# Kernel optimization log

Hardware: AMD Instinct MI355X
Metric: run time of the kernel (lower is better)

The kernel has to match this reference:

```python
import jax, jax.numpy as jnp
import numpy as np

DIM = 1024
HEADS = 16
HEAD_DIM = DIM // HEADS
HIDDEN = 4 * DIM
EPS = 1e-5
SCALE = HEAD_DIM ** -0.5


def _ln(x, g, b):
    m = jnp.mean(x, axis=-1, keepdims=True)
    v = jnp.mean(jnp.square(x - m), axis=-1, keepdims=True)
    return (x - m) * jax.lax.rsqrt(v + EPS) * g + b


def setup_inputs() -> dict:
    key = jax.random.key(0)
    ks = jax.random.split(key, 12)
    B, L = 4, 1024
    s = lambda fan: 1.0 / np.sqrt(fan)
    return {
        "x": jax.random.normal(ks[0], (B, L, DIM), jnp.float32),
        "skip": jax.random.normal(ks[1], (B, L, DIM), jnp.float32),
        "skip_w": jax.random.normal(ks[2], (2 * DIM, DIM), jnp.float32) * s(2 * DIM),
        "skip_b": jnp.zeros((DIM,), jnp.float32),
        "ln1_g": jnp.ones((DIM,), jnp.float32),
        "ln1_b": jnp.zeros((DIM,), jnp.float32),
        "qkv_w": jax.random.normal(ks[3], (DIM, 3 * DIM), jnp.float32) * s(DIM),
        "proj_w": jax.random.normal(ks[4], (DIM, DIM), jnp.float32) * s(DIM),
        "proj_b": jnp.zeros((DIM,), jnp.float32),
        "ln2_g": jnp.ones((DIM,), jnp.float32),
        "ln2_b": jnp.zeros((DIM,), jnp.float32),
        "fc1_w": jax.random.normal(ks[5], (DIM, HIDDEN), jnp.float32) * s(DIM),
        "fc1_b": jnp.zeros((HIDDEN,), jnp.float32),
        "fc2_w": jax.random.normal(ks[6], (HIDDEN, DIM), jnp.float32) * s(HIDDEN),
        "fc2_b": jnp.zeros((DIM,), jnp.float32),
        "ln3_g": jnp.ones((DIM,), jnp.float32),
        "ln3_b": jnp.zeros((DIM,), jnp.float32),
    }


def reference(x, skip, skip_w, skip_b, ln1_g, ln1_b, qkv_w, proj_w, proj_b,
              ln2_g, ln2_b, fc1_w, fc1_b, fc2_w, fc2_b, ln3_g, ln3_b):
    B, L, C = x.shape
    # skip-concat + linear + norm1
    x = jnp.concatenate([x, skip], axis=2) @ skip_w + skip_b
    x = _ln(x, ln1_g, ln1_b)
    # attention (naive: full [B,H,L,L] score matrix, as in source)
    qkv = (x @ qkv_w).reshape(B, L, 3, HEADS, HEAD_DIM)
    qkv = jnp.transpose(qkv, (2, 0, 3, 1, 4))  # [3,B,H,L,D]
    q, k, v = qkv[0], qkv[1], qkv[2]
    attn = jax.nn.softmax(jnp.einsum("bhld,bhmd->bhlm", q, k) * SCALE, axis=-1)
    o = jnp.einsum("bhlm,bhmd->bhld", attn, v)
    o = jnp.transpose(o, (0, 2, 1, 3)).reshape(B, L, C) @ proj_w + proj_b
    x = x + o
    x = _ln(x, ln2_g, ln2_b)
    # MLP with exact (erf) GELU, matching torch default
    h = jax.nn.gelu(x @ fc1_w + fc1_b, approximate=False)
    x = x + (h @ fc2_w + fc2_b)
    x = _ln(x, ln3_g, ln3_b)
    return x
```

## Files before the change

### kernel.cpp

```cpp
#include <hip/hip_runtime.h>

typedef float f32x4 __attribute__((ext_vector_type(4)));
typedef short s16x8 __attribute__((ext_vector_type(8)));

#define MFMA16(a, b, c) __builtin_amdgcn_mfma_f32_16x16x32_bf16(a, b, c, 0, 0, 0)
#define SCALE 0.125f

__device__ __forceinline__ unsigned short f2bf(float f) {
    unsigned u = __float_as_uint(f);
    u = u + 0x7FFFu + ((u >> 16) & 1u);
    return (unsigned short)(u >> 16);
}

__device__ __forceinline__ float fast_gelu(float x) {
    float u = 1.5957691216f * (x + 0.044715f * x * x * x);
    u = fminf(u, 30.f);
    const float e = __expf(u);
    return x * e / (e + 1.f);
}

typedef const __attribute__((address_space(1))) void* gptr_t;
typedef __attribute__((address_space(3))) void* lptr_t;
__device__ __forceinline__ void gload16(const void* g, void* l) {
    __builtin_amdgcn_global_load_lds((gptr_t)g, (lptr_t)l, 16, 0, 0);
}

__global__ __launch_bounds__(256) void cvt_cat(const float* __restrict__ x,
                                               const float* __restrict__ skip,
                                               unsigned short* __restrict__ out) {
    const size_t i = ((size_t)blockIdx.x * 256 + threadIdx.x) * 8;
    const int r = (int)(i >> 11);
    const int c = (int)(i & 2047);
    const float* src = (c < 1024) ? (x + (size_t)r * 1024 + c)
                                  : (skip + (size_t)r * 1024 + (c - 1024));
    float4 v0 = *(const float4*)src;
    float4 v1 = *(const float4*)(src + 4);
    s16x8 o;
    o[0] = f2bf(v0.x); o[1] = f2bf(v0.y); o[2] = f2bf(v0.z); o[3] = f2bf(v0.w);
    o[4] = f2bf(v1.x); o[5] = f2bf(v1.y); o[6] = f2bf(v1.z); o[7] = f2bf(v1.w);
    *(s16x8*)(out + i) = o;
}

__global__ __launch_bounds__(256) void wt_tr(const float* __restrict__ in,
                                             unsigned short* __restrict__ out,
                                             int R, int C) {
    __shared__ unsigned short tile[64][72];
    const int nct = C >> 6;
    const int tr = blockIdx.x / nct, tc = blockIdx.x % nct;
    const int t = threadIdx.x;
    const int r = t >> 2, c0 = (t & 3) << 4;
    const float* src = in + (size_t)(tr * 64 + r) * C + tc * 64 + c0;
#pragma unroll
    for (int j = 0; j < 16; j += 4) {
        float4 v = *(const float4*)(src + j);
        tile[r][c0 + j]     = f2bf(v.x);
        tile[r][c0 + j + 1] = f2bf(v.y);
        tile[r][c0 + j + 2] = f2bf(v.z);
        tile[r][c0 + j + 3] = f2bf(v.w);
    }
    __syncthreads();
    const int oc = t >> 2, r0 = (t & 3) << 4;
    s16x8 o0, o1;
#pragma unroll
    for (int j = 0; j < 8; ++j) { o0[j] = tile[r0 + j][oc]; o1[j] = tile[r0 + 8 + j][oc]; }
    unsigned short* dst = out + (size_t)(tc * 64 + oc) * R + tr * 64 + r0;
    *(s16x8*)dst = o0;
    *(s16x8*)(dst + 8) = o1;
}

__global__ __launch_bounds__(256) void v_transpose(const unsigned short* __restrict__ qkv,
                                                   unsigned short* __restrict__ vt) {
    __shared__ unsigned short tile[64][72];
    const int bh = blockIdx.x >> 4, lt = blockIdx.x & 15;
    const int b = bh >> 4, h = bh & 15;
    const int t = threadIdx.x;
    const int r = t >> 2, c0 = (t & 3) << 4;
    const unsigned short* src =
        qkv + (size_t)(b * 1024 + lt * 64 + r) * 3072 + 2048 + h * 64 + c0;
    s16x8 v0 = *(const s16x8*)src;
    s16x8 v1 = *(const s16x8*)(src + 8);
#pragma unroll
    for (int j = 0; j < 8; ++j) { tile[r][c0 + j] = v0[j]; tile[r][c0 + 8 + j] = v1[j]; }
    __syncthreads();
    const int d = t >> 2, l0 = (t & 3) << 4;
    s16x8 o0, o1;
#pragma unroll
    for (int j = 0; j < 8; ++j) { o0[j] = tile[l0 + j][d]; o1[j] = tile[l0 + 8 + j][d]; }
    unsigned short* dst = vt + (size_t)bh * 65536 + (size_t)d * 1024 + lt * 64 + l0;
    *(s16x8*)dst = o0;
    *(s16x8*)(dst + 8) = o1;
}

__global__ __launch_bounds__(256) void ln_kernel(const float* __restrict__ in,
                                                 const float* __restrict__ g,
                                                 const float* __restrict__ bb,
                                                 float* __restrict__ outf,
                                                 unsigned short* __restrict__ outb) {
    const int row = blockIdx.x;
    const int t = threadIdx.x;
    const float4 v = ((const float4*)(in + (size_t)row * 1024))[t];
    float s = v.x + v.y + v.z + v.w;
    float ss = v.x * v.x + v.y * v.y + v.z * v.z + v.w * v.w;
#pragma unroll
    for (int off = 1; off < 64; off <<= 1) {
        s += __shfl_xor(s, off, 64);
        ss += __shfl_xor(ss, off, 64);
    }
    __shared__ float red[8];
    const int wave = t >> 6, lane = t & 63;
    if (lane == 0) { red[wave] = s; red[4 + wave] = ss; }
    __syncthreads();
    s = red[0] + red[1] + red[2] + red[3];
    ss = red[4] + red[5] + red[6] + red[7];
    const float mean = s * 0.0009765625f;
    const float var = ss * 0.0009765625f - mean * mean;
    const float rstd = rsqrtf(var + 1e-5f);
    const float4 gv = ((const float4*)g)[t];
    const float4 bv = ((const float4*)bb)[t];
    float4 ov;
    ov.x = (v.x - mean) * rstd * gv.x + bv.x;
    ov.y = (v.y - mean) * rstd * gv.y + bv.y;
    ov.z = (v.z - mean) * rstd * gv.z + bv.z;
    ov.w = (v.w - mean) * rstd * gv.w + bv.w;
    if (outf) ((float4*)(outf + (size_t)row * 1024))[t] = ov;
    if (outb) {
        ushort4 ob;
        ob.x = f2bf(ov.x); ob.y = f2bf(ov.y); ob.z = f2bf(ov.z); ob.w = f2bf(ov.w);
        *(ushort4*)(outb + (size_t)row * 1024 + t * 4) = ob;
    }
}

template <int EPI>
__global__ __launch_bounds__(256) void gemm_bt(const unsigned short* __restrict__ A,
                                               const unsigned short* __restrict__ Bt,
                                               void* __restrict__ outp,
                                               const float* __restrict__ bias,
                                               const float* __restrict__ resid,
                                               int M, int N, int K) {
    __shared__ __align__(16) unsigned short sA[2][128 * 32];
    __shared__ __align__(16) unsigned short sB[2][128 * 32];
    const int tid = threadIdx.x, wave = tid >> 6, lane = tid & 63;
    const int fr = lane & 15, fq = lane >> 4;
    const int nbn = N >> 7;
    const int wg = (blockIdx.x & 7) * ((int)gridDim.x >> 3) + (blockIdx.x >> 3);
    const int bm = wg / nbn, bn = wg % nbn;
    const int wm = wave >> 1, wn = wave & 1;
    const unsigned short* Ab = A + (size_t)bm * 128 * K;
    const unsigned short* Bb = Bt + (size_t)bn * 128 * K;
    const int srow = wave * 32 + (lane >> 2);
    const int scol = (lane & 3) * 8;

    f32x4 acc[4][4];
#pragma unroll
    for (int i = 0; i < 4; ++i)
#pragma unroll
        for (int j = 0; j < 4; ++j) acc[i][j] = (f32x4){0.f, 0.f, 0.f, 0.f};

    auto stage = [&](int buf, int k0) {
        const unsigned short* ga = Ab + (size_t)srow * K + k0 + scol;
        const unsigned short* gb = Bb + (size_t)srow * K + k0 + scol;
        unsigned short* la = &sA[buf][wave * 32 * 32];
        unsigned short* lb = &sB[buf][wave * 32 * 32];
        gload16(ga, la);
        gload16(ga + (size_t)16 * K, la + 16 * 32);
        gload16(gb, lb);
        gload16(gb + (size_t)16 * K, lb + 16 * 32);
    };

    const int nkt = K >> 5;
    stage(0, 0);
    for (int kt = 0; kt < nkt; ++kt) {
        __syncthreads();
        if (kt + 1 < nkt) stage((kt + 1) & 1, (kt + 1) * 32);
        const unsigned short* a0 = &sA[kt & 1][0];
        const unsigned short* b0 = &sB[kt & 1][0];
        s16x8 af[4], bf[4];
#pragma unroll
        for (int i = 0; i < 4; ++i)
            af[i] = *(const s16x8*)(a0 + (wm * 64 + i * 16 + fr) * 32 + fq * 8);
#pragma unroll
        for (int j = 0; j < 4; ++j)
            bf[j] = *(const s16x8*)(b0 + (wn * 64 + j * 16 + fr) * 32 + fq * 8);
#pragma unroll
        for (int i = 0; i < 4; ++i)
#pragma unroll
            for (int j = 0; j < 4; ++j) acc[i][j] = MFMA16(af[i], bf[j], acc[i][j]);
    }

#pragma unroll
    for (int i = 0; i < 4; ++i) {
        const int row0 = bm * 128 + wm * 64 + i * 16 + fq * 4;
#pragma unroll
        for (int j = 0; j < 4; ++j) {
            const int col = bn * 128 + wn * 64 + j * 16 + fr;
            const float bv = (EPI == 2) ? 0.f : bias[col];
#pragma unroll
            for (int r = 0; r < 4; ++r) {
                const int row = row0 + r;
                float v = acc[i][j][r] + bv;
                if (EPI == 3) v = fast_gelu(v);
                if (EPI == 1) v += resid[(size_t)row * N + col];
                if (EPI == 0 || EPI == 1)
                    ((float*)outp)[(size_t)row * N + col] = v;
                else
                    ((unsigned short*)outp)[(size_t)row * N + col] = f2bf(v);
            }
        }
    }
}

template <int EPI>
__global__ __launch_bounds__(512) void gemm256(const unsigned short* __restrict__ A,
                                               const unsigned short* __restrict__ Bt,
                                               unsigned short* __restrict__ outp,
                                               const float* __restrict__ bias,
                                               int N, int K) {
    __shared__ __align__(16) unsigned short lds[4][16384];
    const int tid = threadIdx.x, wave = tid >> 6, lane = tid & 63;
    const int fr = lane & 15, fq = lane >> 4;
    const int wm = wave >> 2, wn = wave & 3;
    const int nbn = N >> 8;
    const int wg = (blockIdx.x & 7) * ((int)gridDim.x >> 3) + (blockIdx.x >> 3);
    const int bm = wg / nbn, bn = wg % nbn;
    const unsigned short* Ab = A + (size_t)bm * 256 * K;
    const unsigned short* Bb = Bt + (size_t)bn * 256 * K;
    const int nt = K >> 5;

    f32x4 acc[8][4];
#pragma unroll
    for (int i = 0; i < 8; ++i)
#pragma unroll
        for (int n = 0; n < 4; ++n) acc[i][n] = (f32x4){0.f, 0.f, 0.f, 0.f};

    const int srow = tid >> 2;
    const int scol = (tid & 3) * 8;

    auto stage2 = [&](int tt, int s0) {
#pragma unroll
        for (int s = s0; s < s0 + 2; ++s) {
            const unsigned short* base = (s < 2) ? Ab : Bb;
            const int row = ((s & 1) << 7) + srow;
            gload16(base + (size_t)row * K + tt * 32 + scol,
                    (char*)&lds[tt & 3][0] + s * 8192 + tid * 16);
        }
    };

    stage2(0, 0); stage2(0, 2);
    stage2(1, 0); stage2(1, 2);
    stage2(2, 0); stage2(2, 2);

    for (int t = 0; t < nt; ++t) {
        __builtin_amdgcn_sched_barrier(0);
        if (t + 2 < nt)      asm volatile("s_waitcnt vmcnt(8)" ::: "memory");
        else if (t + 1 < nt) asm volatile("s_waitcnt vmcnt(4)" ::: "memory");
        else                 asm volatile("s_waitcnt vmcnt(0)" ::: "memory");
        __builtin_amdgcn_sched_barrier(0);
        __builtin_amdgcn_s_barrier();

        const unsigned short* lb = &lds[t & 3][0];
        s16x8 af[4], bfr[4];
#pragma unroll
        for (int i = 0; i < 4; ++i)
            af[i] = *(const s16x8*)(lb + (wm * 128 + i * 16 + fr) * 32 + fq * 8);
#pragma unroll
        for (int n = 0; n < 4; ++n)
            bfr[n] = *(const s16x8*)(lb + 8192 + (wn * 64 + n * 16 + fr) * 32 + fq * 8);
        if (t + 3 < nt) stage2(t + 3, 0);
        __builtin_amdgcn_s_barrier();
        __builtin_amdgcn_s_setprio(1);
#pragma unroll
        for (int i = 0; i < 4; ++i)
#pragma unroll
            for (int n = 0; n < 4; ++n) acc[i][n] = MFMA16(af[i], bfr[n], acc[i][n]);
        __builtin_amdgcn_s_setprio(0);
        __builtin_amdgcn_s_barrier();
#pragma unroll
        for (int i = 0; i < 4; ++i)
            af[i] = *(const s16x8*)(lb + (wm * 128 + 64 + i * 16 + fr) * 32 + fq * 8);
        if (t + 3 < nt) stage2(t + 3, 2);
        __builtin_amdgcn_s_barrier();
        __builtin_amdgcn_s_setprio(1);
#pragma unroll
        for (int i = 0; i < 4; ++i)
#pragma unroll
            for (int n = 0; n < 4; ++n) acc[4 + i][n] = MFMA16(af[i], bfr[n], acc[4 + i][n]);
        __builtin_amdgcn_s_setprio(0);
        __builtin_amdgcn_s_barrier();
    }

#pragma unroll
    for (int a2 = 0; a2 < 8; ++a2) {
        const int row0 = bm * 256 + wm * 128 + ((a2 >> 2) << 6) + ((a2 & 3) << 4) + fq * 4;
#pragma unroll
        for (int n = 0; n < 4; ++n) {
            const int col = bn * 256 + wn * 64 + n * 16 + fr;
            const float bv = (EPI == 3) ? bias[col] : 0.f;
#pragma unroll
            for (int r = 0; r < 4; ++r) {
                float v = acc[a2][n][r] + bv;
                if (EPI == 3) v = fast_gelu(v);
                outp[(size_t)(row0 + r) * N + col] = f2bf(v);
            }
        }
    }
}

__global__ __launch_bounds__(256) void attn_kernel(const unsigned short* __restrict__ qkv,
                                                   const unsigned short* __restrict__ vt,
                                                   unsigned short* __restrict__ o) {
    __shared__ __align__(16) unsigned short sK[2][64 * 64];
    __shared__ __align__(16) unsigned short sV[2][64 * 64];
    __shared__ __align__(16) unsigned short sP[4][16 * 64];

    const int j = blockIdx.x;
    const int xcd = j & 7, ix = j >> 3;
    const int bh = xcd * 8 + (ix >> 4);
    const int qt = ix & 15;
    const int b = bh >> 4, h = bh & 15;

    const int tid = threadIdx.x;
    const int wave = tid >> 6, lane = tid & 63;
    const int fr = lane & 15, fq = lane >> 4;

    const unsigned short* kbase = qkv + (size_t)(b * 1024) * 3072 + 1024 + h * 64;
    const unsigned short* vbase = vt + (size_t)bh * 65536;

    const int qrow0 = b * 1024 + qt * 64 + wave * 16;
    const unsigned short* qp = qkv + (size_t)(qrow0 + fr) * 3072 + h * 64;
    const s16x8 aq0 = *(const s16x8*)(qp + fq * 8);
    const s16x8 aq1 = *(const s16x8*)(qp + 32 + fq * 8);

    const f32x4 zero4 = {0.f, 0.f, 0.f, 0.f};
    float m[4], l[4];
    f32x4 oacc[4];
#pragma unroll
    for (int r = 0; r < 4; ++r) { m[r] = -1e30f; l[r] = 0.f; }
#pragma unroll
    for (int n = 0; n < 4; ++n) oacc[n] = zero4;

    auto stage = [&](int buf, int kt) {
#pragma unroll
        for (int c = 0; c < 2; ++c) {
            const int ob = tid * 16 + c * 4096;
            const int row = ob >> 7;
            const int slot = (ob >> 4) & 7;
            const int cole = ((slot ^ (row & 7)) << 3);
            gload16(kbase + (size_t)(kt * 64 + row) * 3072 + cole,
                    (char*)&sK[buf][0] + ob);
            gload16(vbase + (size_t)row * 1024 + kt * 64 + cole,
                    (char*)&sV[buf][0] + ob);
        }
    };

    unsigned short* pw = &sP[wave][0];
    const int psw = (fr & 7) << 4;

    stage(0, 0);
    for (int kt = 0; kt < 16; ++kt) {
        const int cur = kt & 1;
        __syncthreads();
        if (kt + 1 < 16) stage(cur ^ 1, kt + 1);

        const unsigned short* kb = &sK[cur][0];
        f32x4 s[4];
        __builtin_amdgcn_s_setprio(1);
#pragma unroll
        for (int n = 0; n < 4; ++n) {
            const int R = n * 16 + fr;
            const int sw = (R & 7) << 3;
            const s16x8 bk0 = *(const s16x8*)(kb + R * 64 + ((fq * 8) ^ sw));
            const s16x8 bk1 = *(const s16x8*)(kb + R * 64 + ((32 + fq * 8) ^ sw));
            s[n] = MFMA16(aq0, bk0, zero4);
            s[n] = MFMA16(aq1, bk1, s[n]);
        }
        __builtin_amdgcn_s_setprio(0);

        float mnew[4], alpha[4], rs[4];
#pragma unroll
        for (int r = 0; r < 4; ++r) {
            float t = fmaxf(fmaxf(s[0][r], s[1][r]), fmaxf(s[2][r], s[3][r])) * SCALE;
#pragma unroll
            for (int off = 1; off < 16; off <<= 1) t = fmaxf(t, __shfl_xor(t, off, 64));
            mnew[r] = fmaxf(m[r], t);
            alpha[r] = __expf(m[r] - mnew[r]);
            rs[r] = 0.f;
        }
#pragma unroll
        for (int n = 0; n < 4; ++n) {
#pragma unroll
            for (int r = 0; r < 4; ++r) {
                const float p = __expf(s[n][r] * SCALE - mnew[r]);
                rs[r] += p;
                const int prow = fq * 4 + r;
                const int pb = prow * 128 + (((n * 16 + fr) * 2) ^ ((prow & 7) << 4));
                *(unsigned short*)((char*)pw + pb) = f2bf(p);
            }
        }
#pragma unroll
        for (int r = 0; r < 4; ++r) {
            float t = rs[r];
#pragma unroll
            for (int off = 1; off < 16; off <<= 1) t += __shfl_xor(t, off, 64);
            l[r] = l[r] * alpha[r] + t;
            m[r] = mnew[r];
        }
#pragma unroll
        for (int n = 0; n < 4; ++n) {
            oacc[n][0] *= alpha[0]; oacc[n][1] *= alpha[1];
            oacc[n][2] *= alpha[2]; oacc[n][3] *= alpha[3];
        }

        const s16x8 ap0 = *(const s16x8*)((char*)pw + fr * 128 + ((fq * 16) ^ psw));
        const s16x8 ap1 = *(const s16x8*)((char*)pw + fr * 128 + ((64 + fq * 16) ^ psw));
        const unsigned short* vb = &sV[cur][0];
        __builtin_amdgcn_s_setprio(1);
#pragma unroll
        for (int n = 0; n < 4; ++n) {
            const int R = n * 16 + fr;
            const int sw = (R & 7) << 3;
            const s16x8 bv0 = *(const s16x8*)(vb + R * 64 + ((fq * 8) ^ sw));
            const s16x8 bv1 = *(const s16x8*)(vb + R * 64 + ((32 + fq * 8) ^ sw));
            oacc[n] = MFMA16(ap0, bv0, oacc[n]);
            oacc[n] = MFMA16(ap1, bv1, oacc[n]);
        }
        __builtin_amdgcn_s_setprio(0);
    }

#pragma unroll
    for (int r = 0; r < 4; ++r) {
        const float rl = 1.f / l[r];
        const int row = qrow0 + fq * 4 + r;
#pragma unroll
        for (int n = 0; n < 4; ++n) {
            const int col = h * 64 + n * 16 + fr;
            o[(size_t)row * 1024 + col] = f2bf(oacc[n][r] * rl);
        }
    }
}

extern "C" void kernel_launch(void* const* d_in, const int* in_sizes, int n_in,
                              void* d_out, int out_size, void* d_ws, size_t ws_size,
                              hipStream_t stream) {
    (void)in_sizes; (void)n_in; (void)out_size; (void)ws_size;
    const float* x      = (const float*)d_in[0];
    const float* skip   = (const float*)d_in[1];
    const float* skip_w = (const float*)d_in[2];
    const float* skip_b = (const float*)d_in[3];
    const float* ln1_g  = (const float*)d_in[4];
    const float* ln1_b  = (const float*)d_in[5];
    const float* qkv_w  = (const float*)d_in[6];
    const float* proj_w = (const float*)d_in[7];
    const float* proj_b = (const float*)d_in[8];
    const float* ln2_g  = (const float*)d_in[9];
    const float* ln2_b  = (const float*)d_in[10];
    const float* fc1_w  = (const float*)d_in[11];
    const float* fc1_b  = (const float*)d_in[12];
    const float* fc2_w  = (const float*)d_in[13];
    const float* fc2_b  = (const float*)d_in[14];
    const float* ln3_g  = (const float*)d_in[15];
    const float* ln3_b  = (const float*)d_in[16];

    char* ws = (char*)d_ws;
    const size_t MB = 1u << 20;
    unsigned short* skip_wT = (unsigned short*)(ws + 0 * MB);
    unsigned short* qkv_wT  = (unsigned short*)(ws + 4 * MB);
    unsigned short* proj_wT = (unsigned short*)(ws + 10 * MB);
    unsigned short* fc1_wT  = (unsigned short*)(ws + 12 * MB);
    unsigned short* fc2_wT  = (unsigned short*)(ws + 20 * MB);
    float* pre              = (float*)(ws + 28 * MB);
    float* x1               = (float*)(ws + 44 * MB);
    unsigned short* x1b     = (unsigned short*)(ws + 60 * MB);
    unsigned short* qkvb    = (unsigned short*)(ws + 68 * MB);
    float* x2n              = (float*)(ws + 68 * MB);
    unsigned short* x2nb    = (unsigned short*)(ws + 84 * MB);
    unsigned short* vtb     = (unsigned short*)(ws + 92 * MB);
    unsigned short* ob      = (unsigned short*)(ws + 100 * MB);
    unsigned short* hb      = (unsigned short*)(ws + 108 * MB);
    unsigned short* xcatb   = (unsigned short*)(ws + 108 * MB);
    float* outf = (float*)d_out;

    cvt_cat<<<4096, 256, 0, stream>>>(x, skip, xcatb);
    wt_tr<<<512, 256, 0, stream>>>(skip_w, skip_wT, 2048, 1024);
    wt_tr<<<768, 256, 0, stream>>>(qkv_w, qkv_wT, 1024, 3072);
    wt_tr<<<256, 256, 0, stream>>>(proj_w, proj_wT, 1024, 1024);
    wt_tr<<<1024, 256, 0, stream>>>(fc1_w, fc1_wT, 1024, 4096);
    wt_tr<<<1024, 256, 0, stream>>>(fc2_w, fc2_wT, 4096, 1024);

    gemm_bt<0><<<32 * 8, 256, 0, stream>>>(xcatb, skip_wT, pre, skip_b, nullptr, 4096, 1024, 2048);
    ln_kernel<<<4096, 256, 0, stream>>>(pre, ln1_g, ln1_b, x1, x1b);

    gemm256<2><<<192, 512, 0, stream>>>(x1b, qkv_wT, qkvb, nullptr, 3072, 1024);

    v_transpose<<<1024, 256, 0, stream>>>(qkvb, vtb);
    attn_kernel<<<1024, 256, 0, stream>>>(qkvb, vtb, ob);

    gemm_bt<1><<<32 * 8, 256, 0, stream>>>(ob, proj_wT, pre, proj_b, x1, 4096, 1024, 1024);
    ln_kernel<<<4096, 256, 0, stream>>>(pre, ln2_g, ln2_b, x2n, x2nb);

    gemm256<3><<<256, 512, 0, stream>>>(x2nb, fc1_wT, hb, fc1_b, 4096, 1024);

    gemm_bt<1><<<32 * 8, 256, 0, stream>>>(hb, fc2_wT, pre, fc2_b, x2n, 4096, 1024, 4096);
    ln_kernel<<<4096, 256, 0, stream>>>(pre, ln3_g, ln3_b, outf, nullptr);
}
```

Before: 491.5 us.

## Deepen 128-tile GEMM pipeline to 4 LDS stages and XOR-swizzle LDS layout

The 128x128 GEMM used for skip, proj and fc2 moves from double buffering with a full __syncthreads per k-step to a 4-buffer ring, keeping three tiles in flight with explicit vmcnt waits and raised MFMA priority. Both GEMM kernels now XOR-swizzle the 16-byte column slot by row when loading into LDS and when reading fragments, to cut LDS bank conflicts on the fragment reads. This trades more LDS per block and hand-tuned wait counts for better latency hiding.

Result: faster. 433.4 us (-11.8%).

```diff
diff --git a/kernel.cpp b/kernel.cpp
--- a/kernel.cpp
+++ b/kernel.cpp
@@ -131,14 +131,13 @@
 }
 
 template <int EPI>
-__global__ __launch_bounds__(256) void gemm_bt(const unsigned short* __restrict__ A,
-                                               const unsigned short* __restrict__ Bt,
-                                               void* __restrict__ outp,
-                                               const float* __restrict__ bias,
-                                               const float* __restrict__ resid,
-                                               int M, int N, int K) {
-    __shared__ __align__(16) unsigned short sA[2][128 * 32];
-    __shared__ __align__(16) unsigned short sB[2][128 * 32];
+__global__ __launch_bounds__(256) void gemm128p(const unsigned short* __restrict__ A,
+                                                const unsigned short* __restrict__ Bt,
+                                                float* __restrict__ outp,
+                                                const float* __restrict__ bias,
+                                                const float* __restrict__ resid,
+                                                int N, int K) {
+    __shared__ __align__(16) unsigned short lds[4][8192];
     const int tid = threadIdx.x, wave = tid >> 6, lane = tid & 63;
     const int fr = lane & 15, fq = lane >> 4;
     const int nbn = N >> 7;
@@ -147,8 +146,7 @@
     const int wm = wave >> 1, wn = wave & 1;
     const unsigned short* Ab = A + (size_t)bm * 128 * K;
     const unsigned short* Bb = Bt + (size_t)bn * 128 * K;
-    const int srow = wave * 32 + (lane >> 2);
-    const int scol = (lane & 3) * 8;
+    const int nt = K >> 5;
 
     f32x4 acc[4][4];
 #pragma unroll
@@ -156,35 +154,42 @@
 #pragma unroll
         for (int j = 0; j < 4; ++j) acc[i][j] = (f32x4){0.f, 0.f, 0.f, 0.f};
 
-    auto stage = [&](int buf, int k0) {
-        const unsigned short* ga = Ab + (size_t)srow * K + k0 + scol;
-        const unsigned short* gb = Bb + (size_t)srow * K + k0 + scol;
-        unsigned short* la = &sA[buf][wave * 32 * 32];
-        unsigned short* lb = &sB[buf][wave * 32 * 32];
-        gload16(ga, la);
-        gload16(ga + (size_t)16 * K, la + 16 * 32);
-        gload16(gb, lb);
-        gload16(gb + (size_t)16 * K, lb + 16 * 32);
+    const int r0 = tid >> 2, slot = tid & 3;
+    auto stage = [&](int tt) {
+        char* dst = (char*)&lds[tt & 3][0];
+#pragma unroll
+        for (int h = 0; h < 2; ++h) {
+            const int row = r0 + h * 64;
+            const int cole = ((slot ^ (row & 3)) << 3);
+            gload16(Ab + (size_t)row * K + tt * 32 + cole, dst + h * 4096 + tid * 16);
+            gload16(Bb + (size_t)row * K + tt * 32 + cole, dst + 8192 + h * 4096 + tid * 16);
+        }
     };
 
-    const int nkt = K >> 5;
-    stage(0, 0);
-    for (int kt = 0; kt < nkt; ++kt) {
-        __syncthreads();
-        if (kt + 1 < nkt) stage((kt + 1) & 1, (kt + 1) * 32);
-        const unsigned short* a0 = &sA[kt & 1][0];
-        const unsigned short* b0 = &sB[kt & 1][0];
-        s16x8 af[4], bf[4];
+    stage(0); stage(1); stage(2);
+    for (int t = 0; t < nt; ++t) {
+        __builtin_amdgcn_sched_barrier(0);
+        if (t + 2 < nt)      asm volatile("s_waitcnt vmcnt(8)" ::: "memory");
+        else if (t + 1 < nt) asm volatile("s_waitcnt vmcnt(4)" ::: "memory");
+        else                 asm volatile("s_waitcnt vmcnt(0)" ::: "memory");
+        __builtin_amdgcn_sched_barrier(0);
+        __builtin_amdgcn_s_barrier();
+
+        const unsigned short* lb = &lds[t & 3][0];
+        s16x8 af[4], bfr[4];
 #pragma unroll
         for (int i = 0; i < 4; ++i)
-            af[i] = *(const s16x8*)(a0 + (wm * 64 + i * 16 + fr) * 32 + fq * 8);
+            af[i] = *(const s16x8*)(lb + (wm * 64 + i * 16 + fr) * 32 + ((fq ^ (fr & 3)) << 3));
 #pragma unroll
         for (int j = 0; j < 4; ++j)
-            bf[j] = *(const s16x8*)(b0 + (wn * 64 + j * 16 + fr) * 32 + fq * 8);
+            bfr[j] = *(const s16x8*)(lb + 4096 + (wn * 64 + j * 16 + fr) * 32 + ((fq ^ (fr & 3)) << 3));
+        if (t + 3 < nt) stage(t + 3);
+        __builtin_amdgcn_s_setprio(1);
 #pragma unroll
         for (int i = 0; i < 4; ++i)
 #pragma unroll
-            for (int j = 0; j < 4; ++j) acc[i][j] = MFMA16(af[i], bf[j], acc[i][j]);
+            for (int j = 0; j < 4; ++j) acc[i][j] = MFMA16(af[i], bfr[j], acc[i][j]);
+        __builtin_amdgcn_s_setprio(0);
     }
 
 #pragma unroll
@@ -193,17 +198,13 @@
 #pragma unroll
         for (int j = 0; j < 4; ++j) {
             const int col = bn * 128 + wn * 64 + j * 16 + fr;
-            const float bv = (EPI == 2) ? 0.f : bias[col];
+            const float bv = bias[col];
 #pragma unroll
             for (int r = 0; r < 4; ++r) {
                 const int row = row0 + r;
                 float v = acc[i][j][r] + bv;
-                if (EPI == 3) v = fast_gelu(v);
                 if (EPI == 1) v += resid[(size_t)row * N + col];
-                if (EPI == 0 || EPI == 1)
-                    ((float*)outp)[(size_t)row * N + col] = v;
-                else
-                    ((unsigned short*)outp)[(size_t)row * N + col] = f2bf(v);
+                outp[(size_t)row * N + col] = v;
             }
         }
     }
@@ -233,14 +234,14 @@
         for (int n = 0; n < 4; ++n) acc[i][n] = (f32x4){0.f, 0.f, 0.f, 0.f};
 
     const int srow = tid >> 2;
-    const int scol = (tid & 3) * 8;
+    const int scole = (((tid & 3) ^ (srow & 3)) << 3);
 
     auto stage2 = [&](int tt, int s0) {
 #pragma unroll
         for (int s = s0; s < s0 + 2; ++s) {
             const unsigned short* base = (s < 2) ? Ab : Bb;
             const int row = ((s & 1) << 7) + srow;
-            gload16(base + (size_t)row * K + tt * 32 + scol,
+            gload16(base + (size_t)row * K + tt * 32 + scole,
                     (char*)&lds[tt & 3][0] + s * 8192 + tid * 16);
         }
     };
@@ -259,12 +260,13 @@
 
         const unsigned short* lb = &lds[t & 3][0];
         s16x8 af[4], bfr[4];
+        const int rsw = (fq ^ (fr & 3)) << 3;
 #pragma unroll
         for (int i = 0; i < 4; ++i)
-            af[i] = *(const s16x8*)(lb + (wm * 128 + i * 16 + fr) * 32 + fq * 8);
+            af[i] = *(const s16x8*)(lb + (wm * 128 + i * 16 + fr) * 32 + rsw);
 #pragma unroll
         for (int n = 0; n < 4; ++n)
-            bfr[n] = *(const s16x8*)(lb + 8192 + (wn * 64 + n * 16 + fr) * 32 + fq * 8);
+            bfr[n] = *(const s16x8*)(lb + 8192 + (wn * 64 + n * 16 + fr) * 32 + rsw);
         if (t + 3 < nt) stage2(t + 3, 0);
         __builtin_amdgcn_s_barrier();
         __builtin_amdgcn_s_setprio(1);
@@ -276,7 +278,7 @@
         __builtin_amdgcn_s_barrier();
 #pragma unroll
         for (int i = 0; i < 4; ++i)
-            af[i] = *(const s16x8*)(lb + (wm * 128 + 64 + i * 16 + fr) * 32 + fq * 8);
+            af[i] = *(const s16x8*)(lb + (wm * 128 + 64 + i * 16 + fr) * 32 + rsw);
         if (t + 3 < nt) stage2(t + 3, 2);
         __builtin_amdgcn_s_barrier();
         __builtin_amdgcn_s_setprio(1);
@@ -486,7 +488,7 @@
     wt_tr<<<1024, 256, 0, stream>>>(fc1_w, fc1_wT, 1024, 4096);
     wt_tr<<<1024, 256, 0, stream>>>(fc2_w, fc2_wT, 4096, 1024);
 
-    gemm_bt<0><<<32 * 8, 256, 0, stream>>>(xcatb, skip_wT, pre, skip_b, nullptr, 4096, 1024, 2048);
+    gemm128p<0><<<256, 256, 0, stream>>>(xcatb, skip_wT, pre, skip_b, nullptr, 1024, 2048);
     ln_kernel<<<4096, 256, 0, stream>>>(pre, ln1_g, ln1_b, x1, x1b);
 
     gemm256<2><<<192, 512, 0, stream>>>(x1b, qkv_wT, qkvb, nullptr, 3072, 1024);
@@ -494,11 +496,11 @@
     v_transpose<<<1024, 256, 0, stream>>>(qkvb, vtb);
     attn_kernel<<<1024, 256, 0, stream>>>(qkvb, vtb, ob);
 
-    gemm_bt<1><<<32 * 8, 256, 0, stream>>>(ob, proj_wT, pre, proj_b, x1, 4096, 1024, 1024);
+    gemm128p<1><<<256, 256, 0, stream>>>(ob, proj_wT, pre, proj_b, x1, 1024, 1024);
     ln_kernel<<<4096, 256, 0, stream>>>(pre, ln2_g, ln2_b, x2n, x2nb);
 
     gemm256<3><<<256, 512, 0, stream>>>(x2nb, fc1_wT, hb, fc1_b, 4096, 1024);
 
-    gemm_bt<1><<<32 * 8, 256, 0, stream>>>(hb, fc2_wT, pre, fc2_b, x2n, 4096, 1024, 4096);
+    gemm128p<1><<<256, 256, 0, stream>>>(hb, fc2_wT, pre, fc2_b, x2n, 1024, 4096);
     ln_kernel<<<4096, 256, 0, stream>>>(pre, ln3_g, ln3_b, outf, nullptr);
 }
```
